# Kernel optimization log

Measured on AMD Instinct MI355X. Metric: run time of the kernel, lower is better.

## Reference

```python
import jax, jax.numpy as jnp
import numpy as np


def setup_inputs() -> dict:
    key = jax.random.key(0)
    k1, k2 = jax.random.split(key)
    b, n, m, d = 16, 2048, 2048, 512
    q = jax.random.normal(k1, (b, n, d), dtype=jnp.float32)
    k = jax.random.normal(k2, (b, m, d), dtype=jnp.float32)
    return {"q": q, "k": k}


def reference(q, k):
    # q: [b, n, d], k: [b, m, d]
    dim = q.shape[-1]
    scale = dim ** (-0.5)
    # scores: [b, n, m]
    scores = jnp.einsum("bnd,bmd->bnm", q, k) * scale
    return jax.nn.softmax(scores, axis=-1)
```

## Files before the change

kernel.cpp:

```cpp
#include <hip/hip_runtime.h>
#include <hip/hip_fp16.h>
#include <math.h>

#define BATCH 16
#define NQ 2048
#define NK 2048
#define DIM 512
#define QK_SCALE 0.044194173824159216f

#define BM 128
#define BN 128
#define BK 32

typedef _Float16 f16x8 __attribute__((ext_vector_type(8)));
typedef _Float16 f16x4 __attribute__((ext_vector_type(4)));
typedef float f32x4 __attribute__((ext_vector_type(4)));

__global__ __launch_bounds__(256) void convert_f32_to_f16(
    const float4* __restrict__ q, const float4* __restrict__ k,
    f16x4* __restrict__ qh, f16x4* __restrict__ kh, int n4_each)
{
    int stride = gridDim.x * blockDim.x;
    for (int i = blockIdx.x * blockDim.x + threadIdx.x; i < 2 * n4_each; i += stride) {
        float4 v;
        f16x4* dst;
        if (i < n4_each) { v = q[i]; dst = qh + i; }
        else             { v = k[i - n4_each]; dst = kh + (i - n4_each); }
        f16x4 o;
        o[0] = (_Float16)v.x; o[1] = (_Float16)v.y;
        o[2] = (_Float16)v.z; o[3] = (_Float16)v.w;
        *dst = o;
    }
}

__global__ __launch_bounds__(256, 2) void qk_exp_gemm(
    const _Float16* __restrict__ qh, const _Float16* __restrict__ kh,
    float* __restrict__ out, float* __restrict__ rowsum)
{
    __shared__ _Float16 As[2][BM * BK];
    __shared__ _Float16 Bs[2][BN * BK];

    const int tid  = threadIdx.x;
    const int lane = tid & 63;
    const int w    = tid >> 6;
    const int wr   = w >> 1;
    const int wc   = w & 1;
    const int bz   = blockIdx.z;
    const int brow = blockIdx.y * BM;
    const int bcol = blockIdx.x * BN;

    const _Float16* qbase = qh + (size_t)(bz * NQ + brow) * DIM;
    const _Float16* kbase = kh + (size_t)(bz * NK + bcol) * DIM;

    const int lr = lane & 15;
    const int ls = lane >> 4;

    auto stage = [&](int buf, int t) {
        const int k0 = t * BK;
#pragma unroll
        for (int i = 0; i < 2; ++i) {
            const int c    = w * 2 + i;
            const int row  = c * 16 + (lane >> 2);
            const int slot = lane & 3;
            const _Float16* ga = qbase + row * DIM + k0 + slot * 8;
            const _Float16* gb = kbase + row * DIM + k0 + slot * 8;
            __builtin_amdgcn_global_load_lds(
                (const __attribute__((address_space(1))) void*)ga,
                (__attribute__((address_space(3))) void*)&As[buf][c * 512 + lane * 8],
                16, 0, 0);
            __builtin_amdgcn_global_load_lds(
                (const __attribute__((address_space(1))) void*)gb,
                (__attribute__((address_space(3))) void*)&Bs[buf][c * 512 + lane * 8],
                16, 0, 0);
        }
    };

    f32x4 acc[4][4] = {};

    stage(0, 0);
    __syncthreads();

    const int NT = DIM / BK;
    for (int t = 0; t < NT; ++t) {
        const int buf = t & 1;
        if (t + 1 < NT) stage(buf ^ 1, t + 1);

        f16x8 a[4], b[4];
#pragma unroll
        for (int mi = 0; mi < 4; ++mi) {
            const int r = wr * 64 + mi * 16 + lr;
            a[mi] = *(const f16x8*)&As[buf][r * BK + ls * 8];
        }
#pragma unroll
        for (int nj = 0; nj < 4; ++nj) {
            const int c = wc * 64 + nj * 16 + lr;
            b[nj] = *(const f16x8*)&Bs[buf][c * BK + ls * 8];
        }
#pragma unroll
        for (int mi = 0; mi < 4; ++mi)
#pragma unroll
            for (int nj = 0; nj < 4; ++nj)
                acc[mi][nj] = __builtin_amdgcn_mfma_f32_16x16x32_f16(
                    a[mi], b[nj], acc[mi][nj], 0, 0, 0);

        __syncthreads();
    }

    float* outb = out + (size_t)bz * NQ * NK;
#pragma unroll
    for (int mi = 0; mi < 4; ++mi) {
#pragma unroll
        for (int r = 0; r < 4; ++r) {
            const int rowl = wr * 64 + mi * 16 + ls * 4 + r;
            const int grow = brow + rowl;
            float psum = 0.f;
#pragma unroll
            for (int nj = 0; nj < 4; ++nj) {
                const int gcol = bcol + wc * 64 + nj * 16 + lr;
                float p = expf(acc[mi][nj][r] * QK_SCALE);
                psum += p;
                outb[(size_t)grow * NK + gcol] = p;
            }
#pragma unroll
            for (int off = 1; off < 16; off <<= 1)
                psum += __shfl_xor(psum, off, 64);
            if (lr == 0)
                atomicAdd(&rowsum[bz * NQ + grow], psum);
        }
    }
}

__global__ __launch_bounds__(256) void softmax_norm(
    float4* __restrict__ out, const float* __restrict__ rowsum, int n4)
{
    int stride = gridDim.x * blockDim.x;
    for (int i = blockIdx.x * blockDim.x + threadIdx.x; i < n4; i += stride) {
        const int row = i >> 9;
        const float inv = 1.0f / rowsum[row];
        float4 v = out[i];
        v.x *= inv; v.y *= inv; v.z *= inv; v.w *= inv;
        out[i] = v;
    }
}

extern "C" void kernel_launch(void* const* d_in, const int* in_sizes, int n_in,
                              void* d_out, int out_size, void* d_ws, size_t ws_size,
                              hipStream_t stream)
{
    const float* q = (const float*)d_in[0];
    const float* k = (const float*)d_in[1];
    float* out = (float*)d_out;

    const size_t elems = (size_t)BATCH * NQ * DIM;
    _Float16* qh = (_Float16*)d_ws;
    _Float16* kh = qh + elems;
    float* rowsum = (float*)(kh + elems);

    hipMemsetAsync(rowsum, 0, BATCH * NQ * sizeof(float), stream);

    const int n4_each = (int)(elems / 4);
    convert_f32_to_f16<<<2048, 256, 0, stream>>>(
        (const float4*)q, (const float4*)k, (f16x4*)qh, (f16x4*)kh, n4_each);

    dim3 grid(NK / BN, NQ / BM, BATCH);
    qk_exp_gemm<<<grid, 256, 0, stream>>>(qh, kh, out, rowsum);

    const int n4o = (int)((size_t)BATCH * NQ * NK / 4);
    softmax_norm<<<2048, 256, 0, stream>>>((float4*)out, rowsum, n4o);
}
```

Baseline: 572.8 us.

## Store unnormalized exp scores as fp16 intermediate and swizzle block order

Measured after the change: 530.7 us. -7.3%, faster.

```diff
diff --git a/kernel.cpp b/kernel.cpp
--- a/kernel.cpp
+++ b/kernel.cpp
@@ -6,7 +6,7 @@
 #define NQ 2048
 #define NK 2048
 #define DIM 512
-#define QK_SCALE 0.044194173824159216f
+#define EXP2_SCALE (0.044194173824159216f * 1.4426950408889634f)
 
 #define BM 128
 #define BN 128
@@ -35,7 +35,7 @@
 
 __global__ __launch_bounds__(256, 2) void qk_exp_gemm(
     const _Float16* __restrict__ qh, const _Float16* __restrict__ kh,
-    float* __restrict__ out, float* __restrict__ rowsum)
+    _Float16* __restrict__ ph, float* __restrict__ rowsum)
 {
     __shared__ _Float16 As[2][BM * BK];
     __shared__ _Float16 Bs[2][BN * BK];
@@ -46,8 +46,11 @@
     const int wr   = w >> 1;
     const int wc   = w & 1;
     const int bz   = blockIdx.z;
-    const int brow = blockIdx.y * BM;
-    const int bcol = blockIdx.x * BN;
+
+    const int lin = blockIdx.y * 16 + blockIdx.x;
+    const int swz = (lin & 7) * 32 + (lin >> 3);
+    const int brow = (swz >> 4) * BM;
+    const int bcol = (swz & 15) * BN;
 
     const _Float16* qbase = qh + (size_t)(bz * NQ + brow) * DIM;
     const _Float16* kbase = kh + (size_t)(bz * NK + bcol) * DIM;
@@ -106,7 +109,7 @@
         __syncthreads();
     }
 
-    float* outb = out + (size_t)bz * NQ * NK;
+    _Float16* pb = ph + (size_t)bz * NQ * NK;
 #pragma unroll
     for (int mi = 0; mi < 4; ++mi) {
 #pragma unroll
@@ -117,9 +120,9 @@
 #pragma unroll
             for (int nj = 0; nj < 4; ++nj) {
                 const int gcol = bcol + wc * 64 + nj * 16 + lr;
-                float p = expf(acc[mi][nj][r] * QK_SCALE);
+                float p = __builtin_amdgcn_exp2f(acc[mi][nj][r] * EXP2_SCALE);
                 psum += p;
-                outb[(size_t)grow * NK + gcol] = p;
+                pb[(size_t)grow * NK + gcol] = (_Float16)p;
             }
 #pragma unroll
             for (int off = 1; off < 16; off <<= 1)
@@ -131,15 +134,21 @@
 }
 
 __global__ __launch_bounds__(256) void softmax_norm(
-    float4* __restrict__ out, const float* __restrict__ rowsum, int n4)
+    const f16x8* __restrict__ ph, const float* __restrict__ rowsum,
+    float4* __restrict__ out, int n8)
 {
     int stride = gridDim.x * blockDim.x;
-    for (int i = blockIdx.x * blockDim.x + threadIdx.x; i < n4; i += stride) {
-        const int row = i >> 9;
+    for (int i = blockIdx.x * blockDim.x + threadIdx.x; i < n8; i += stride) {
+        const int row = i >> 8;
         const float inv = 1.0f / rowsum[row];
-        float4 v = out[i];
-        v.x *= inv; v.y *= inv; v.z *= inv; v.w *= inv;
-        out[i] = v;
+        f16x8 v = ph[i];
+        float4 o0, o1;
+        o0.x = (float)v[0] * inv; o0.y = (float)v[1] * inv;
+        o0.z = (float)v[2] * inv; o0.w = (float)v[3] * inv;
+        o1.x = (float)v[4] * inv; o1.y = (float)v[5] * inv;
+        o1.z = (float)v[6] * inv; o1.w = (float)v[7] * inv;
+        out[i * 2]     = o0;
+        out[i * 2 + 1] = o1;
     }
 }
 
@@ -152,9 +161,11 @@
     float* out = (float*)d_out;
 
     const size_t elems = (size_t)BATCH * NQ * DIM;
+    const size_t pelems = (size_t)BATCH * NQ * NK;
     _Float16* qh = (_Float16*)d_ws;
     _Float16* kh = qh + elems;
-    float* rowsum = (float*)(kh + elems);
+    _Float16* ph = kh + elems;
+    float* rowsum = (float*)(ph + pelems);
 
     hipMemsetAsync(rowsum, 0, BATCH * NQ * sizeof(float), stream);
 
@@ -163,8 +174,9 @@
         (const float4*)q, (const float4*)k, (f16x4*)qh, (f16x4*)kh, n4_each);
 
     dim3 grid(NK / BN, NQ / BM, BATCH);
-    qk_exp_gemm<<<grid, 256, 0, stream>>>(qh, kh, out, rowsum);
+    qk_exp_gemm<<<grid, 256, 0, stream>>>(qh, kh, ph, rowsum);
 
-    const int n4o = (int)((size_t)BATCH * NQ * NK / 4);
-    softmax_norm<<<2048, 256, 0, stream>>>((float4*)out, rowsum, n4o);
+    const int n8 = (int)(pelems / 8);
+    softmax_norm<<<2048, 256, 0, stream>>>(
+        (const f16x8*)ph, rowsum, (float4*)out, n8);
 }
```
